# Kernel tuning notes

Hardware: AMD Instinct MI355X
Metric: run time of the kernel (lower is better)

## Reference

```python
import jax, jax.numpy as jnp
import numpy as np

N1, N2, K = 262144, 65536, 16   # dense points, coarse points, knn neighbors
CIN, COUT = 64, 64              # in_planes, out_planes
EPS = 1e-5


def bn(x, g, b, m, v):
    # eval-mode BatchNorm1d with learned affine and running stats
    return (x - m) * jax.lax.rsqrt(v + EPS) * g + b


def setup_inputs() -> dict:
    key = jax.random.key(0)
    ks = jax.random.split(key, 32)
    u = lambda k, *s: jax.random.normal(k, s, jnp.float32)
    lin = lambda k, o, i: jax.random.normal(k, (o, i), jnp.float32) / np.float32(np.sqrt(i))
    inp = dict(
        p1=u(ks[0], N1, 3), p2=u(ks[1], N2, 3),
        x1=u(ks[2], N1, COUT), x2=u(ks[3], N2, CIN),
        knn_idx=jax.random.randint(ks[4], (N2, K), 0, N1),
        # linear1: Linear(COUT,COUT) + BN + ReLU
        w1=lin(ks[5], COUT, COUT), b1=0.01 * u(ks[6], COUT),
        g1=jnp.ones(COUT), be1=jnp.zeros(COUT),
        m1=0.1 * u(ks[7], COUT), v1=jax.random.uniform(ks[8], (COUT,), minval=0.5, maxval=1.5),
        # linear2: Linear(CIN,COUT) + BN + ReLU
        w2=lin(ks[9], COUT, CIN), b2=0.01 * u(ks[10], COUT),
        g2=jnp.ones(COUT), be2=jnp.zeros(COUT),
        m2=0.1 * u(ks[11], COUT), v2=jax.random.uniform(ks[12], (COUT,), minval=0.5, maxval=1.5),
        # channel_shrinker: Linear(CIN+3,CIN) + BN + ReLU + Linear(CIN,1)
        ws1=lin(ks[13], CIN, CIN + 3), bs1=0.01 * u(ks[14], CIN),
        gs=jnp.ones(CIN), bes=jnp.zeros(CIN),
        ms=0.1 * u(ks[15], CIN), vs=jax.random.uniform(ks[16], (CIN,), minval=0.5, maxval=1.5),
        ws2=lin(ks[17], 1, CIN), bs2=0.01 * u(ks[18], 1),
    )
    return inp


def reference(p1, p2, x1, x2, knn_idx,
              w1, b1, g1, be1, m1, v1,
              w2, b2, g2, be2, m2, v2,
              ws1, bs1, gs, bes, ms, vs, ws2, bs2):
    idx = knn_idx.reshape(-1)                                   # [M] = [N2*K], indices into p1
    # relative position of each knn neighbor to its coarse query point
    p_r = p1[idx].reshape(N2, K, 3) - p2[:, None, :]            # [N2,K,3]
    x2k = jnp.concatenate(
        [p_r, jnp.broadcast_to(x2[:, None, :], (N2, K, CIN))], axis=-1
    ).reshape(N2 * K, CIN + 3)                                  # [M, CIN+3]
    # channel_shrinker MLP -> scalar logit per (coarse, neighbor) pair
    h = jax.nn.relu(bn(x2k @ ws1.T + bs1, gs, bes, ms, vs))     # [M, CIN]
    logit = (h @ ws2.T + bs2)[:, 0]                             # [M]
    # scatter_softmax over variable in-degree groups keyed by dense point idx
    gmax = jax.lax.stop_gradient(jax.ops.segment_max(logit, idx, num_segments=N1))
    e = jnp.exp(logit - gmax[idx])
    denom = jax.ops.segment_sum(e, idx, num_segments=N1)
    prob = e / denom[idx]                                       # [M]
    # linear2(x2), broadcast over K neighbors, weight, scatter-sum to dense points
    up_feat = jax.nn.relu(bn(x2 @ w2.T + b2, g2, be2, m2, v2))  # [N2, COUT]
    weighted = (up_feat[:, None, :] * prob.reshape(N2, K, 1)).reshape(N2 * K, COUT)
    up = jax.ops.segment_sum(weighted, idx, num_segments=N1)    # [N1, COUT]
    # skip branch: linear1(x1)
    y1 = jax.nn.relu(bn(x1 @ w1.T + b1, g1, be1, m1, v1))       # [N1, COUT]
    return y1 + up
```

## Files before the change

kernel.cpp:

```cpp
#include <hip/hip_runtime.h>

#define CN1 262144
#define CN2 65536
#define CK  16
#define CM  (CN2*CK)

typedef unsigned short u16;
typedef unsigned int   u32;
typedef float f32x4 __attribute__((ext_vector_type(4)));

__device__ __forceinline__ float b2f(u16 h) {
    union { u32 u; float f; } v; v.u = ((u32)h) << 16; return v.f;
}
__device__ __forceinline__ u16 f2b(float f) {
    union { float f; u32 u; } v; v.f = f;
    u32 lsb = (v.u >> 16) & 1u;
    return (u16)((v.u + 0x7FFFu + lsb) >> 16);
}

#define W_POS   0
#define W_FT    256
#define W_AS    12544
#define W_BS    12608
#define W_WS2   12672
#define W_A2    12736
#define W_B2    12800
#define W_A1    12864
#define W_B1    12928
#define W_BS2   12992
#define W_MODE  13000
#define W_W1T   13056
#define W_W2T   17152

__device__ __forceinline__ float ldv(const void* p, size_t i, int bf) {
    return bf ? b2f(((const u16*)p)[i]) : ((const float*)p)[i];
}

#define DECL_ACC \
    f32x4 A0={0,0,0,0},A1={0,0,0,0},A2={0,0,0,0},A3={0,0,0,0}, \
          A4={0,0,0,0},A5={0,0,0,0},A6={0,0,0,0},A7={0,0,0,0}, \
          A8={0,0,0,0},A9={0,0,0,0},A10={0,0,0,0},A11={0,0,0,0}, \
          A12={0,0,0,0},A13={0,0,0,0},A14={0,0,0,0},A15={0,0,0,0};

#define FMA4(A, Wv) \
    (A).x = fmaf(xv_, (Wv).x, (A).x); (A).y = fmaf(xv_, (Wv).y, (A).y); \
    (A).z = fmaf(xv_, (Wv).z, (A).z); (A).w = fmaf(xv_, (Wv).w, (A).w);

#define WSTEP(wt, ivar, xval) { \
    float xv_ = (xval); \
    const f32x4* wr_ = (const f32x4*)((wt) + ((size_t)(ivar) << 6)); \
    FMA4(A0, wr_[0])   FMA4(A1, wr_[1])   FMA4(A2, wr_[2])   FMA4(A3, wr_[3]) \
    FMA4(A4, wr_[4])   FMA4(A5, wr_[5])   FMA4(A6, wr_[6])   FMA4(A7, wr_[7]) \
    FMA4(A8, wr_[8])   FMA4(A9, wr_[9])   FMA4(A10,wr_[10])  FMA4(A11,wr_[11]) \
    FMA4(A12,wr_[12])  FMA4(A13,wr_[13])  FMA4(A14,wr_[14])  FMA4(A15,wr_[15]) }

#define GEMV64T(bf, xrow_f, xrow_u4, wt) \
    if (bf) { \
        const uint4* xu_ = (xrow_u4); \
        _Pragma("unroll 2") \
        for (int ii_ = 0; ii_ < 8; ++ii_) { \
            uint4 xc_ = xu_[ii_]; \
            WSTEP(wt, ii_*8+0, b2f((u16)(xc_.x & 0xffffu))) \
            WSTEP(wt, ii_*8+1, b2f((u16)(xc_.x >> 16))) \
            WSTEP(wt, ii_*8+2, b2f((u16)(xc_.y & 0xffffu))) \
            WSTEP(wt, ii_*8+3, b2f((u16)(xc_.y >> 16))) \
            WSTEP(wt, ii_*8+4, b2f((u16)(xc_.z & 0xffffu))) \
            WSTEP(wt, ii_*8+5, b2f((u16)(xc_.z >> 16))) \
            WSTEP(wt, ii_*8+6, b2f((u16)(xc_.w & 0xffffu))) \
            WSTEP(wt, ii_*8+7, b2f((u16)(xc_.w >> 16))) \
        } \
    } else { \
        const float4* xf_ = (xrow_f); \
        _Pragma("unroll 2") \
        for (int ii_ = 0; ii_ < 8; ++ii_) { \
            float4 xa_ = xf_[2*ii_], xb_ = xf_[2*ii_+1]; \
            WSTEP(wt, ii_*8+0, xa_.x) WSTEP(wt, ii_*8+1, xa_.y) \
            WSTEP(wt, ii_*8+2, xa_.z) WSTEP(wt, ii_*8+3, xa_.w) \
            WSTEP(wt, ii_*8+4, xb_.x) WSTEP(wt, ii_*8+5, xb_.y) \
            WSTEP(wt, ii_*8+6, xb_.z) WSTEP(wt, ii_*8+7, xb_.w) \
        } \
    }

#define BNR1(A, av, bv) \
    (A).x = fmaxf(fmaf((A).x,(av).x,(bv).x),0.f); \
    (A).y = fmaxf(fmaf((A).y,(av).y,(bv).y),0.f); \
    (A).z = fmaxf(fmaf((A).z,(av).z,(bv).z),0.f); \
    (A).w = fmaxf(fmaf((A).w,(av).w,(bv).w),0.f);
#define BNR_ALL(aBase, bBase) { \
    const f32x4* av_ = (const f32x4*)(aBase); \
    const f32x4* bv_ = (const f32x4*)(bBase); \
    BNR1(A0,av_[0],bv_[0])   BNR1(A1,av_[1],bv_[1]) \
    BNR1(A2,av_[2],bv_[2])   BNR1(A3,av_[3],bv_[3]) \
    BNR1(A4,av_[4],bv_[4])   BNR1(A5,av_[5],bv_[5]) \
    BNR1(A6,av_[6],bv_[6])   BNR1(A7,av_[7],bv_[7]) \
    BNR1(A8,av_[8],bv_[8])   BNR1(A9,av_[9],bv_[9]) \
    BNR1(A10,av_[10],bv_[10]) BNR1(A11,av_[11],bv_[11]) \
    BNR1(A12,av_[12],bv_[12]) BNR1(A13,av_[13],bv_[13]) \
    BNR1(A14,av_[14],bv_[14]) BNR1(A15,av_[15],bv_[15]) }

#define UFQ(q, AL, AH) { uint4 u_ = ufr_[q]; \
    (AL).x = fmaf(pe_, b2f((u16)(u_.x & 0xffffu)), (AL).x); \
    (AL).y = fmaf(pe_, b2f((u16)(u_.x >> 16)),     (AL).y); \
    (AL).z = fmaf(pe_, b2f((u16)(u_.y & 0xffffu)), (AL).z); \
    (AL).w = fmaf(pe_, b2f((u16)(u_.y >> 16)),     (AL).w); \
    (AH).x = fmaf(pe_, b2f((u16)(u_.z & 0xffffu)), (AH).x); \
    (AH).y = fmaf(pe_, b2f((u16)(u_.z >> 16)),     (AH).y); \
    (AH).z = fmaf(pe_, b2f((u16)(u_.w & 0xffffu)), (AH).z); \
    (AH).w = fmaf(pe_, b2f((u16)(u_.w >> 16)),     (AH).w); }

#define STQ(q, AL, AH, dst) { uint4 o_; \
    o_.x = (u32)f2b((AL).x) | ((u32)f2b((AL).y) << 16); \
    o_.y = (u32)f2b((AL).z) | ((u32)f2b((AL).w) << 16); \
    o_.z = (u32)f2b((AH).x) | ((u32)f2b((AH).y) << 16); \
    o_.w = (u32)f2b((AH).z) | ((u32)f2b((AH).w) << 16); \
    ((uint4*)(dst))[q] = o_; }
#define STORE_BF(dst) \
    STQ(0,A0,A1,dst)  STQ(1,A2,A3,dst)  STQ(2,A4,A5,dst)  STQ(3,A6,A7,dst) \
    STQ(4,A8,A9,dst)  STQ(5,A10,A11,dst) STQ(6,A12,A13,dst) STQ(7,A14,A15,dst)
#define STORE_F32(dst) { f32x4* ov_ = (f32x4*)(dst); \
    ov_[0]=A0;  ov_[1]=A1;  ov_[2]=A2;  ov_[3]=A3; \
    ov_[4]=A4;  ov_[5]=A5;  ov_[6]=A6;  ov_[7]=A7; \
    ov_[8]=A8;  ov_[9]=A9;  ov_[10]=A10;ov_[11]=A11; \
    ov_[12]=A12;ov_[13]=A13;ov_[14]=A14;ov_[15]=A15; }

__global__ __launch_bounds__(256) void k_prep(
    const void* __restrict__ w1,  const void* __restrict__ b1,  const void* __restrict__ g1,
    const void* __restrict__ be1, const void* __restrict__ m1,  const void* __restrict__ v1,
    const void* __restrict__ w2,  const void* __restrict__ b2,  const void* __restrict__ g2,
    const void* __restrict__ be2, const void* __restrict__ m2,  const void* __restrict__ v2,
    const void* __restrict__ ws1, const void* __restrict__ bs1, const void* __restrict__ gs,
    const void* __restrict__ bes, const void* __restrict__ ms,  const void* __restrict__ vs,
    const void* __restrict__ ws2, const void* __restrict__ bs2, float* __restrict__ wb,
    u32* __restrict__ offsets, u32* __restrict__ cursor)
{
    int b = blockIdx.x;
    int tid = threadIdx.x;
    if (b > 0) {
        offsets[(b - 1) * 256 + tid] = 0u;
        if (b == 1 && tid == 0) *cursor = 0u;
        return;
    }

    u32 w0 = ((const u32*)g1)[0];
    int bf = (w0 != 0x3F800000u) ? 1 : 0;

    for (int t = tid; t < 64*64; t += 256) {
        int i = t >> 6, c = t & 63;
        wb[W_FT  + t] = ldv(ws1, (size_t)c*67 + 3 + i, bf);
        wb[W_W1T + t] = ldv(w1,  (size_t)c*64 + i, bf);
        wb[W_W2T + t] = ldv(w2,  (size_t)c*64 + i, bf);
    }
    for (int t = tid; t < 64*3; t += 256) {
        int j = t / 3, k = t % 3;
        wb[W_POS + t] = ldv(ws1, (size_t)j*67 + k, bf);
    }
    if (tid < 64) {
        float as = ldv(gs, tid, bf) * rsqrtf(ldv(vs, tid, bf) + 1e-5f);
        wb[W_AS + tid] = as;
        wb[W_BS + tid] = (ldv(bs1, tid, bf) - ldv(ms, tid, bf)) * as + ldv(bes, tid, bf);
        wb[W_WS2 + tid] = ldv(ws2, tid, bf);
        float a2 = ldv(g2, tid, bf) * rsqrtf(ldv(v2, tid, bf) + 1e-5f);
        wb[W_A2 + tid] = a2;
        wb[W_B2 + tid] = (ldv(b2, tid, bf) - ldv(m2, tid, bf)) * a2 + ldv(be2, tid, bf);
        float a1 = ldv(g1, tid, bf) * rsqrtf(ldv(v1, tid, bf) + 1e-5f);
        wb[W_A1 + tid] = a1;
        wb[W_B1 + tid] = (ldv(b1, tid, bf) - ldv(m1, tid, bf)) * a1 + ldv(be1, tid, bf);
    }
    if (tid == 0) {
        wb[W_BS2] = ldv(bs2, 0, bf);
        ((u32*)wb)[W_MODE] = (u32)bf;
    }
}

__global__ __launch_bounds__(256, 4) void k_coarse2(
    const void* __restrict__ x2, const int* __restrict__ knn,
    const float* __restrict__ wb,
    float* __restrict__ dots, u16* __restrict__ upfeat,
    u32* __restrict__ offsets)
{
    int bf   = (int)((const u32*)wb)[W_MODE];
    int role = blockIdx.x & 1;
    int n2   = (blockIdx.x >> 1) * 256 + threadIdx.x;
    const float4* xf = (const float4*)((const float*)x2 + (size_t)n2 * 64);
    const uint4*  xu = (const uint4*)((const u16*)x2 + (size_t)n2 * 64);

    if (role == 0) {
        const int4* kv = (const int4*)(knn + (size_t)n2 * 16);
        #pragma unroll
        for (int q = 0; q < 4; q++) {
            int4 t = kv[q];
            atomicAdd(&offsets[t.x & (CN1-1)], 1u);
            atomicAdd(&offsets[t.y & (CN1-1)], 1u);
            atomicAdd(&offsets[t.z & (CN1-1)], 1u);
            atomicAdd(&offsets[t.w & (CN1-1)], 1u);
        }
        DECL_ACC
        GEMV64T(bf, xf, xu, wb + W_FT)
        STORE_F32(dots + (size_t)n2 * 64)
    } else {
        DECL_ACC
        GEMV64T(bf, xf, xu, wb + W_W2T)
        BNR_ALL(wb + W_A2, wb + W_B2)
        STORE_BF(upfeat + (size_t)n2 * 64)
    }
}

__global__ __launch_bounds__(256) void k_scan(
    u32* __restrict__ offsets, u32* __restrict__ cursor)
{
    __shared__ u32 s[256];
    __shared__ u32 base;
    int t = threadIdx.x;
    int i = blockIdx.x * 256 + t;
    u32 v = offsets[i];
    s[t] = v; __syncthreads();
    for (int off = 1; off < 256; off <<= 1) {
        u32 add = (t >= off) ? s[t-off] : 0u;
        __syncthreads();
        s[t] += add;
        __syncthreads();
    }
    u32 inc = s[t];
    if (t == 255) base = atomicAdd(cursor, inc);
    __syncthreads();
    offsets[i] = (base + inc - v) << 6;
}

__global__ __launch_bounds__(256) void k_logit_scatter(
    const void* __restrict__ p1, const void* __restrict__ p2,
    const int* __restrict__ knn, const float* __restrict__ wb,
    const float* __restrict__ dots,
    float* __restrict__ logits, u32* __restrict__ offsets,
    u32* __restrict__ csr)
{
    int bf = (int)((const u32*)wb)[W_MODE];
    int m  = blockIdx.x * 256 + threadIdx.x;
    int n2 = m >> 4;

    int idx = knn[m] & (CN1-1);

    u32 v = atomicAdd(&offsets[idx], 1u);
    u32 pos = (v >> 6) + (v & 63u);
    csr[pos & (CM-1)] = (u32)m;

    float prx = ldv(p1, (size_t)idx*3+0, bf) - ldv(p2, (size_t)n2*3+0, bf);
    float pry = ldv(p1, (size_t)idx*3+1, bf) - ldv(p2, (size_t)n2*3+1, bf);
    float prz = ldv(p1, (size_t)idx*3+2, bf) - ldv(p2, (size_t)n2*3+2, bf);

    const float* dr = dots + (size_t)n2 * 64;
    float lg = 0.f;
    #pragma unroll 8
    for (int j = 0; j < 64; ++j) {
        float pre = fmaf(prz, wb[W_POS + j*3+2],
                    fmaf(pry, wb[W_POS + j*3+1],
                    fmaf(prx, wb[W_POS + j*3+0], dr[j])));
        float h = fmaxf(fmaf(pre, wb[W_AS+j], wb[W_BS+j]), 0.f);
        lg = fmaf(h, wb[W_WS2+j], lg);
    }
    logits[m] = lg + wb[W_BS2];
}

__global__ __launch_bounds__(256, 4) void k_dense(
    const void* __restrict__ x1, const float* __restrict__ wb,
    const float* __restrict__ logits, const u16* __restrict__ upfeat,
    const u32* __restrict__ offsets, const u32* __restrict__ csr,
    void* __restrict__ out)
{
    int bf = (int)((const u32*)wb)[W_MODE];
    int n1 = blockIdx.x * 256 + threadIdx.x;

    u32 pk = offsets[n1];
    int d = (int)(pk & 63u);
    int start = (int)(pk >> 6);

    float mxv = -3.0e38f, s = 0.f;
    for (int e = 0; e < d; ++e) {
        u32 m = csr[(u32)(start + e) & (CM-1)] & (CM-1);
        float l = logits[m];
        float mnew = fmaxf(mxv, l);
        s = fmaf(s, __expf(mxv - mnew), __expf(l - mnew));
        mxv = mnew;
    }
    float inv = (d > 0) ? (1.f / s) : 0.f;

    DECL_ACC
    GEMV64T(bf, (const float4*)((const float*)x1 + (size_t)n1 * 64),
                (const uint4*)((const u16*)x1 + (size_t)n1 * 64),
                wb + W_W1T)
    BNR_ALL(wb + W_A1, wb + W_B1)

    for (int e = 0; e < d; ++e) {
        u32 m = csr[(u32)(start + e) & (CM-1)] & (CM-1);
        float pe_ = __expf(logits[m] - mxv) * inv;
        const uint4* ufr_ = (const uint4*)(upfeat + (size_t)(m >> 4) * 64);
        UFQ(0,A0,A1)   UFQ(1,A2,A3)   UFQ(2,A4,A5)   UFQ(3,A6,A7)
        UFQ(4,A8,A9)   UFQ(5,A10,A11) UFQ(6,A12,A13) UFQ(7,A14,A15)
    }

    if (bf) { u16* orow = (u16*)out + (size_t)n1 * 64; STORE_BF(orow) }
    else    { STORE_F32((float*)out + (size_t)n1 * 64) }
}

extern "C" void kernel_launch(void* const* d_in, const int* in_sizes, int n_in,
                              void* d_out, int out_size, void* d_ws, size_t ws_size,
                              hipStream_t stream)
{
    (void)in_sizes; (void)n_in; (void)out_size; (void)ws_size;
    const void* p1   = d_in[0];
    const void* p2   = d_in[1];
    const void* x1   = d_in[2];
    const void* x2   = d_in[3];
    const int*  knn  = (const int*)d_in[4];
    const void* w1   = d_in[5];
    const void* b1   = d_in[6];
    const void* g1   = d_in[7];
    const void* be1  = d_in[8];
    const void* m1   = d_in[9];
    const void* v1   = d_in[10];
    const void* w2   = d_in[11];
    const void* b2   = d_in[12];
    const void* g2   = d_in[13];
    const void* be2  = d_in[14];
    const void* m2   = d_in[15];
    const void* v2   = d_in[16];
    const void* ws1  = d_in[17];
    const void* bs1  = d_in[18];
    const void* gs   = d_in[19];
    const void* bes  = d_in[20];
    const void* ms   = d_in[21];
    const void* vs   = d_in[22];
    const void* ws2w = d_in[23];
    const void* bs2  = d_in[24];

    char* ws = (char*)d_ws;
    float* wb      = (float*)(ws);
    float* logits  = (float*)(ws + ((size_t)1  << 20));
    u32*   csr     = (u32*)  (ws + ((size_t)5  << 20));
    u16*   upfeat  = (u16*)  (ws + ((size_t)9  << 20));
    u32*   offsets = (u32*)  (ws + ((size_t)17 << 20));
    u32*   cursor  = (u32*)  (ws + ((size_t)18 << 20));
    float* dots    = (float*)d_out;

    k_prep          <<<1 + CN1/256, 256, 0, stream>>>(w1,b1,g1,be1,m1,v1,
                                                      w2,b2,g2,be2,m2,v2,
                                                      ws1,bs1,gs,bes,ms,vs,
                                                      ws2w, bs2, wb, offsets, cursor);
    k_coarse2       <<<2*(CN2/256), 256, 0, stream>>>(x2, knn, wb, dots, upfeat, offsets);
    k_scan          <<<CN1/256,     256, 0, stream>>>(offsets, cursor);
    k_logit_scatter <<<CM/256,      256, 0, stream>>>(p1, p2, knn, wb, dots,
                                                      logits, offsets, csr);
    k_dense         <<<CN1/256,     256, 0, stream>>>(x1, wb, logits, upfeat,
                                                      offsets, csr, d_out);
}
```

Before: 232.6 us.

## Split output channels across thread pairs and pack logit weights for vector loads

```diff
diff --git a/kernel.cpp b/kernel.cpp
--- a/kernel.cpp
+++ b/kernel.cpp
@@ -31,53 +31,50 @@
 #define W_MODE  13000
 #define W_W1T   13056
 #define W_W2T   17152
+#define W_JP    21248
 
 __device__ __forceinline__ float ldv(const void* p, size_t i, int bf) {
     return bf ? b2f(((const u16*)p)[i]) : ((const float*)p)[i];
 }
 
-#define DECL_ACC \
+#define DECL_ACC8 \
     f32x4 A0={0,0,0,0},A1={0,0,0,0},A2={0,0,0,0},A3={0,0,0,0}, \
-          A4={0,0,0,0},A5={0,0,0,0},A6={0,0,0,0},A7={0,0,0,0}, \
-          A8={0,0,0,0},A9={0,0,0,0},A10={0,0,0,0},A11={0,0,0,0}, \
-          A12={0,0,0,0},A13={0,0,0,0},A14={0,0,0,0},A15={0,0,0,0};
+          A4={0,0,0,0},A5={0,0,0,0},A6={0,0,0,0},A7={0,0,0,0};
 
 #define FMA4(A, Wv) \
     (A).x = fmaf(xv_, (Wv).x, (A).x); (A).y = fmaf(xv_, (Wv).y, (A).y); \
     (A).z = fmaf(xv_, (Wv).z, (A).z); (A).w = fmaf(xv_, (Wv).w, (A).w);
 
-#define WSTEP(wt, ivar, xval) { \
+#define WSTEP8(wtco, ivar, xval) { \
     float xv_ = (xval); \
-    const f32x4* wr_ = (const f32x4*)((wt) + ((size_t)(ivar) << 6)); \
-    FMA4(A0, wr_[0])   FMA4(A1, wr_[1])   FMA4(A2, wr_[2])   FMA4(A3, wr_[3]) \
-    FMA4(A4, wr_[4])   FMA4(A5, wr_[5])   FMA4(A6, wr_[6])   FMA4(A7, wr_[7]) \
-    FMA4(A8, wr_[8])   FMA4(A9, wr_[9])   FMA4(A10,wr_[10])  FMA4(A11,wr_[11]) \
-    FMA4(A12,wr_[12])  FMA4(A13,wr_[13])  FMA4(A14,wr_[14])  FMA4(A15,wr_[15]) }
-
-#define GEMV64T(bf, xrow_f, xrow_u4, wt) \
+    const f32x4* wr_ = (const f32x4*)((wtco) + ((size_t)(ivar) << 6)); \
+    FMA4(A0, wr_[0])  FMA4(A1, wr_[1])  FMA4(A2, wr_[2])  FMA4(A3, wr_[3]) \
+    FMA4(A4, wr_[4])  FMA4(A5, wr_[5])  FMA4(A6, wr_[6])  FMA4(A7, wr_[7]) }
+
+#define GEMV32T(bf, xrow_f, xrow_u4, wtco) \
     if (bf) { \
         const uint4* xu_ = (xrow_u4); \
         _Pragma("unroll 2") \
         for (int ii_ = 0; ii_ < 8; ++ii_) { \
             uint4 xc_ = xu_[ii_]; \
-            WSTEP(wt, ii_*8+0, b2f((u16)(xc_.x & 0xffffu))) \
-            WSTEP(wt, ii_*8+1, b2f((u16)(xc_.x >> 16))) \
-            WSTEP(wt, ii_*8+2, b2f((u16)(xc_.y & 0xffffu))) \
-            WSTEP(wt, ii_*8+3, b2f((u16)(xc_.y >> 16))) \
-            WSTEP(wt, ii_*8+4, b2f((u16)(xc_.z & 0xffffu))) \
-            WSTEP(wt, ii_*8+5, b2f((u16)(xc_.z >> 16))) \
-            WSTEP(wt, ii_*8+6, b2f((u16)(xc_.w & 0xffffu))) \
-            WSTEP(wt, ii_*8+7, b2f((u16)(xc_.w >> 16))) \
+            WSTEP8(wtco, ii_*8+0, b2f((u16)(xc_.x & 0xffffu))) \
+            WSTEP8(wtco, ii_*8+1, b2f((u16)(xc_.x >> 16))) \
+            WSTEP8(wtco, ii_*8+2, b2f((u16)(xc_.y & 0xffffu))) \
+            WSTEP8(wtco, ii_*8+3, b2f((u16)(xc_.y >> 16))) \
+            WSTEP8(wtco, ii_*8+4, b2f((u16)(xc_.z & 0xffffu))) \
+            WSTEP8(wtco, ii_*8+5, b2f((u16)(xc_.z >> 16))) \
+            WSTEP8(wtco, ii_*8+6, b2f((u16)(xc_.w & 0xffffu))) \
+            WSTEP8(wtco, ii_*8+7, b2f((u16)(xc_.w >> 16))) \
         } \
     } else { \
         const float4* xf_ = (xrow_f); \
         _Pragma("unroll 2") \
         for (int ii_ = 0; ii_ < 8; ++ii_) { \
             float4 xa_ = xf_[2*ii_], xb_ = xf_[2*ii_+1]; \
-            WSTEP(wt, ii_*8+0, xa_.x) WSTEP(wt, ii_*8+1, xa_.y) \
-            WSTEP(wt, ii_*8+2, xa_.z) WSTEP(wt, ii_*8+3, xa_.w) \
-            WSTEP(wt, ii_*8+4, xb_.x) WSTEP(wt, ii_*8+5, xb_.y) \
-            WSTEP(wt, ii_*8+6, xb_.z) WSTEP(wt, ii_*8+7, xb_.w) \
+            WSTEP8(wtco, ii_*8+0, xa_.x) WSTEP8(wtco, ii_*8+1, xa_.y) \
+            WSTEP8(wtco, ii_*8+2, xa_.z) WSTEP8(wtco, ii_*8+3, xa_.w) \
+            WSTEP8(wtco, ii_*8+4, xb_.x) WSTEP8(wtco, ii_*8+5, xb_.y) \
+            WSTEP8(wtco, ii_*8+6, xb_.z) WSTEP8(wtco, ii_*8+7, xb_.w) \
         } \
     }
 
@@ -86,17 +83,13 @@
     (A).y = fmaxf(fmaf((A).y,(av).y,(bv).y),0.f); \
     (A).z = fmaxf(fmaf((A).z,(av).z,(bv).z),0.f); \
     (A).w = fmaxf(fmaf((A).w,(av).w,(bv).w),0.f);
-#define BNR_ALL(aBase, bBase) { \
+#define BNR8(aBase, bBase) { \
     const f32x4* av_ = (const f32x4*)(aBase); \
     const f32x4* bv_ = (const f32x4*)(bBase); \
-    BNR1(A0,av_[0],bv_[0])   BNR1(A1,av_[1],bv_[1]) \
-    BNR1(A2,av_[2],bv_[2])   BNR1(A3,av_[3],bv_[3]) \
-    BNR1(A4,av_[4],bv_[4])   BNR1(A5,av_[5],bv_[5]) \
-    BNR1(A6,av_[6],bv_[6])   BNR1(A7,av_[7],bv_[7]) \
-    BNR1(A8,av_[8],bv_[8])   BNR1(A9,av_[9],bv_[9]) \
-    BNR1(A10,av_[10],bv_[10]) BNR1(A11,av_[11],bv_[11]) \
-    BNR1(A12,av_[12],bv_[12]) BNR1(A13,av_[13],bv_[13]) \
-    BNR1(A14,av_[14],bv_[14]) BNR1(A15,av_[15],bv_[15]) }
+    BNR1(A0,av_[0],bv_[0]) BNR1(A1,av_[1],bv_[1]) \
+    BNR1(A2,av_[2],bv_[2]) BNR1(A3,av_[3],bv_[3]) \
+    BNR1(A4,av_[4],bv_[4]) BNR1(A5,av_[5],bv_[5]) \
+    BNR1(A6,av_[6],bv_[6]) BNR1(A7,av_[7],bv_[7]) }
 
 #define UFQ(q, AL, AH) { uint4 u_ = ufr_[q]; \
     (AL).x = fmaf(pe_, b2f((u16)(u_.x & 0xffffu)), (AL).x); \
@@ -114,14 +107,11 @@
     o_.z = (u32)f2b((AH).x) | ((u32)f2b((AH).y) << 16); \
     o_.w = (u32)f2b((AH).z) | ((u32)f2b((AH).w) << 16); \
     ((uint4*)(dst))[q] = o_; }
-#define STORE_BF(dst) \
-    STQ(0,A0,A1,dst)  STQ(1,A2,A3,dst)  STQ(2,A4,A5,dst)  STQ(3,A6,A7,dst) \
-    STQ(4,A8,A9,dst)  STQ(5,A10,A11,dst) STQ(6,A12,A13,dst) STQ(7,A14,A15,dst)
-#define STORE_F32(dst) { f32x4* ov_ = (f32x4*)(dst); \
-    ov_[0]=A0;  ov_[1]=A1;  ov_[2]=A2;  ov_[3]=A3; \
-    ov_[4]=A4;  ov_[5]=A5;  ov_[6]=A6;  ov_[7]=A7; \
-    ov_[8]=A8;  ov_[9]=A9;  ov_[10]=A10;ov_[11]=A11; \
-    ov_[12]=A12;ov_[13]=A13;ov_[14]=A14;ov_[15]=A15; }
+#define STORE_BF8(dst) \
+    STQ(0,A0,A1,dst) STQ(1,A2,A3,dst) STQ(2,A4,A5,dst) STQ(3,A6,A7,dst)
+#define STORE_F328(dst) { f32x4* ov_ = (f32x4*)(dst); \
+    ov_[0]=A0; ov_[1]=A1; ov_[2]=A2; ov_[3]=A3; \
+    ov_[4]=A4; ov_[5]=A5; ov_[6]=A6; ov_[7]=A7; }
 
 __global__ __launch_bounds__(256) void k_prep(
     const void* __restrict__ w1,  const void* __restrict__ b1,  const void* __restrict__ g1,
@@ -156,15 +146,25 @@
     }
     if (tid < 64) {
         float as = ldv(gs, tid, bf) * rsqrtf(ldv(vs, tid, bf) + 1e-5f);
+        float bs = (ldv(bs1, tid, bf) - ldv(ms, tid, bf)) * as + ldv(bes, tid, bf);
+        float wc = ldv(ws2, tid, bf);
         wb[W_AS + tid] = as;
-        wb[W_BS + tid] = (ldv(bs1, tid, bf) - ldv(ms, tid, bf)) * as + ldv(bes, tid, bf);
-        wb[W_WS2 + tid] = ldv(ws2, tid, bf);
+        wb[W_BS + tid] = bs;
+        wb[W_WS2 + tid] = wc;
         float a2 = ldv(g2, tid, bf) * rsqrtf(ldv(v2, tid, bf) + 1e-5f);
         wb[W_A2 + tid] = a2;
         wb[W_B2 + tid] = (ldv(b2, tid, bf) - ldv(m2, tid, bf)) * a2 + ldv(be2, tid, bf);
         float a1 = ldv(g1, tid, bf) * rsqrtf(ldv(v1, tid, bf) + 1e-5f);
         wb[W_A1 + tid] = a1;
         wb[W_B1 + tid] = (ldv(b1, tid, bf) - ldv(m1, tid, bf)) * a1 + ldv(be1, tid, bf);
+        wb[W_JP + tid*8 + 0] = ldv(ws1, (size_t)tid*67 + 0, bf);
+        wb[W_JP + tid*8 + 1] = ldv(ws1, (size_t)tid*67 + 1, bf);
+        wb[W_JP + tid*8 + 2] = ldv(ws1, (size_t)tid*67 + 2, bf);
+        wb[W_JP + tid*8 + 3] = as;
+        wb[W_JP + tid*8 + 4] = bs;
+        wb[W_JP + tid*8 + 5] = wc;
+        wb[W_JP + tid*8 + 6] = 0.f;
+        wb[W_JP + tid*8 + 7] = 0.f;
     }
     if (tid == 0) {
         wb[W_BS2] = ldv(bs2, 0, bf);
@@ -172,36 +172,39 @@
     }
 }
 
-__global__ __launch_bounds__(256, 4) void k_coarse2(
+__global__ __launch_bounds__(256, 8) void k_coarse2(
     const void* __restrict__ x2, const int* __restrict__ knn,
     const float* __restrict__ wb,
     float* __restrict__ dots, u16* __restrict__ upfeat,
     u32* __restrict__ offsets)
 {
     int bf   = (int)((const u32*)wb)[W_MODE];
+    int tid  = threadIdx.x;
     int role = blockIdx.x & 1;
-    int n2   = (blockIdx.x >> 1) * 256 + threadIdx.x;
+    int n2   = (blockIdx.x >> 1) * 128 + (tid >> 1);
+    int half = tid & 1;
+    int co   = half << 5;
     const float4* xf = (const float4*)((const float*)x2 + (size_t)n2 * 64);
     const uint4*  xu = (const uint4*)((const u16*)x2 + (size_t)n2 * 64);
 
     if (role == 0) {
         const int4* kv = (const int4*)(knn + (size_t)n2 * 16);
         #pragma unroll
-        for (int q = 0; q < 4; q++) {
-            int4 t = kv[q];
+        for (int q = 0; q < 2; q++) {
+            int4 t = kv[half*2 + q];
             atomicAdd(&offsets[t.x & (CN1-1)], 1u);
             atomicAdd(&offsets[t.y & (CN1-1)], 1u);
             atomicAdd(&offsets[t.z & (CN1-1)], 1u);
             atomicAdd(&offsets[t.w & (CN1-1)], 1u);
         }
-        DECL_ACC
-        GEMV64T(bf, xf, xu, wb + W_FT)
-        STORE_F32(dots + (size_t)n2 * 64)
+        DECL_ACC8
+        GEMV32T(bf, xf, xu, wb + W_FT + co)
+        STORE_F328(dots + (size_t)n2 * 64 + co)
     } else {
-        DECL_ACC
-        GEMV64T(bf, xf, xu, wb + W_W2T)
-        BNR_ALL(wb + W_A2, wb + W_B2)
-        STORE_BF(upfeat + (size_t)n2 * 64)
+        DECL_ACC8
+        GEMV32T(bf, xf, xu, wb + W_W2T + co)
+        BNR8(wb + W_A2 + co, wb + W_B2 + co)
+        STORE_BF8(upfeat + (size_t)n2 * 64 + co)
     }
 }
 
@@ -226,6 +229,11 @@
     offsets[i] = (base + inc - v) << 6;
 }
 
+#define LSTEP(j, dv) { f32x4 pa_ = jp[2*(j)], pb_ = jp[2*(j)+1]; \
+    float pre_ = fmaf(prz, pa_.z, fmaf(pry, pa_.y, fmaf(prx, pa_.x, (dv)))); \
+    float h_ = fmaxf(fmaf(pre_, pa_.w, pb_.x), 0.f); \
+    lg = fmaf(h_, pb_.y, lg); }
+
 __global__ __launch_bounds__(256) void k_logit_scatter(
     const void* __restrict__ p1, const void* __restrict__ p2,
     const int* __restrict__ knn, const float* __restrict__ wb,
@@ -247,27 +255,28 @@
     float pry = ldv(p1, (size_t)idx*3+1, bf) - ldv(p2, (size_t)n2*3+1, bf);
     float prz = ldv(p1, (size_t)idx*3+2, bf) - ldv(p2, (size_t)n2*3+2, bf);
 
-    const float* dr = dots + (size_t)n2 * 64;
+    const f32x4*  jp  = (const f32x4*)(wb + W_JP);
+    const float4* dr4 = (const float4*)(dots + (size_t)n2 * 64);
     float lg = 0.f;
-    #pragma unroll 8
-    for (int j = 0; j < 64; ++j) {
-        float pre = fmaf(prz, wb[W_POS + j*3+2],
-                    fmaf(pry, wb[W_POS + j*3+1],
-                    fmaf(prx, wb[W_POS + j*3+0], dr[j])));
-        float h = fmaxf(fmaf(pre, wb[W_AS+j], wb[W_BS+j]), 0.f);
-        lg = fmaf(h, wb[W_WS2+j], lg);
+    #pragma unroll 4
+    for (int jq = 0; jq < 16; ++jq) {
+        float4 d4 = dr4[jq];
+        LSTEP(jq*4+0, d4.x) LSTEP(jq*4+1, d4.y)
+        LSTEP(jq*4+2, d4.z) LSTEP(jq*4+3, d4.w)
     }
     logits[m] = lg + wb[W_BS2];
 }
 
-__global__ __launch_bounds__(256, 4) void k_dense(
+__global__ __launch_bounds__(256, 8) void k_dense(
     const void* __restrict__ x1, const float* __restrict__ wb,
     const float* __restrict__ logits, const u16* __restrict__ upfeat,
     const u32* __restrict__ offsets, const u32* __restrict__ csr,
     void* __restrict__ out)
 {
-    int bf = (int)((const u32*)wb)[W_MODE];
-    int n1 = blockIdx.x * 256 + threadIdx.x;
+    int bf  = (int)((const u32*)wb)[W_MODE];
+    int tid = threadIdx.x;
+    int n1  = blockIdx.x * 128 + (tid >> 1);
+    int co  = (tid & 1) << 5;
 
     u32 pk = offsets[n1];
     int d = (int)(pk & 63u);
@@ -283,22 +292,21 @@
     }
     float inv = (d > 0) ? (1.f / s) : 0.f;
 
-    DECL_ACC
-    GEMV64T(bf, (const float4*)((const float*)x1 + (size_t)n1 * 64),
+    DECL_ACC8
+    GEMV32T(bf, (const float4*)((const float*)x1 + (size_t)n1 * 64),
                 (const uint4*)((const u16*)x1 + (size_t)n1 * 64),
-                wb + W_W1T)
-    BNR_ALL(wb + W_A1, wb + W_B1)
+                wb + W_W1T + co)
+    BNR8(wb + W_A1 + co, wb + W_B1 + co)
 
     for (int e = 0; e < d; ++e) {
         u32 m = csr[(u32)(start + e) & (CM-1)] & (CM-1);
         float pe_ = __expf(logits[m] - mxv) * inv;
-        const uint4* ufr_ = (const uint4*)(upfeat + (size_t)(m >> 4) * 64);
-        UFQ(0,A0,A1)   UFQ(1,A2,A3)   UFQ(2,A4,A5)   UFQ(3,A6,A7)
-        UFQ(4,A8,A9)   UFQ(5,A10,A11) UFQ(6,A12,A13) UFQ(7,A14,A15)
-    }
-
-    if (bf) { u16* orow = (u16*)out + (size_t)n1 * 64; STORE_BF(orow) }
-    else    { STORE_F32((float*)out + (size_t)n1 * 64) }
+        const uint4* ufr_ = (const uint4*)(upfeat + (size_t)(m >> 4) * 64 + co);
+        UFQ(0,A0,A1) UFQ(1,A2,A3) UFQ(2,A4,A5) UFQ(3,A6,A7)
+    }
+
+    if (bf) { u16* orow = (u16*)out + (size_t)n1 * 64 + co; STORE_BF8(orow) }
+    else    { STORE_F328((float*)out + (size_t)n1 * 64 + co) }
 }
 
 extern "C" void kernel_launch(void* const* d_in, const int* in_sizes, int n_in,
@@ -345,10 +353,10 @@
                                                       w2,b2,g2,be2,m2,v2,
                                                       ws1,bs1,gs,bes,ms,vs,
                                                       ws2w, bs2, wb, offsets, cursor);
-    k_coarse2       <<<2*(CN2/256), 256, 0, stream>>>(x2, knn, wb, dots, upfeat, offsets);
+    k_coarse2       <<<2*(CN2/128), 256, 0, stream>>>(x2, knn, wb, dots, upfeat, offsets);
     k_scan          <<<CN1/256,     256, 0, stream>>>(offsets, cursor);
     k_logit_scatter <<<CM/256,      256, 0, stream>>>(p1, p2, knn, wb, dots,
                                                       logits, offsets, csr);
-    k_dense         <<<CN1/256,     256, 0, stream>>>(x1, wb, logits, upfeat,
+    k_dense         <<<CN1/128,     256, 0, stream>>>(x1, wb, logits, upfeat,
                                                       offsets, csr, d_out);
 }
```

Result: slower. 552.5 us (+137.5%).
